# Kernel optimization log

Hardware: AMD Instinct MI355X
Metric: run time of the kernel (lower is better)

The kernel has to match this reference:

```python
import jax, jax.numpy as jnp
import numpy as np

N = 50000
E = 800000
H = 128

def setup_inputs() -> dict:
    key = jax.random.key(0)
    ks = jax.random.split(key, 12)
    s = 1.0 / np.sqrt(H)
    inp = {
        "x": jax.random.normal(ks[0], (N, H), dtype=jnp.float32),
        "edge_index": jax.random.randint(ks[1], (2, E), 0, N, dtype=jnp.int64),
        "edge_attr": jax.random.normal(ks[2], (E, H), dtype=jnp.float32),
        # linear_edge: Linear(3H, H)
        "We": jax.random.uniform(ks[3], (3 * H, H), jnp.float32, -s, s),
        "be": jnp.zeros((H,), jnp.float32),
        # attention_layer.W: Linear(H, H)
        "Wg": jax.random.uniform(ks[4], (H, H), jnp.float32, -s, s),
        "bg": jnp.zeros((H,), jnp.float32),
        # attention_layer.a: Linear(2H, 1)
        "Wa": jax.random.uniform(ks[5], (2 * H, 1), jnp.float32, -s, s),
        "ba": jnp.zeros((1,), jnp.float32),
        # linear_out: Linear(H, H)
        "Wo": jax.random.uniform(ks[6], (H, H), jnp.float32, -s, s),
        "bo": jnp.zeros((H,), jnp.float32),
    }
    return inp


def reference(x, edge_index, edge_attr, We, be, Wg, bg, Wa, ba, Wo, bo):
    # PyG MessagePassing (flow=source_to_target): j = edge_index[0] (source),
    # i = edge_index[1] (target); aggregation scatters to edge_index[1].
    src = edge_index[0]
    dst = edge_index[1]

    # message: SiLU(Linear(cat[x_i, x_j, edge_attr]))  -- split We to avoid a [E,3H] concat
    m = jax.nn.silu(x[dst] @ We[:H] + x[src] @ We[H:2 * H] + edge_attr @ We[2 * H:] + be)  # [E,H]
    agg = jax.ops.segment_sum(m, dst, num_segments=N)  # [N,H] scatter-add aggregate

    # GraphAttentionLayer: row, col = edge_index -> row=edge_index[0], col=edge_index[1]
    h = agg @ Wg + bg  # [N,H]
    score = jax.nn.leaky_relu(h[src] @ Wa[:H] + h[dst] @ Wa[H:] + ba, negative_slope=0.2)  # [E,1]
    # softmax over the last dim of size 1 -> all ones (faithful to original); dropout off (eval)
    alpha = jax.nn.softmax(score, axis=-1)  # [E,1]
    attn_out = jax.ops.segment_sum(alpha * h[dst], src, num_segments=N)  # [N,H]

    return attn_out @ Wo + bo  # linear_out
```

## Files before the change

### kernel.cpp

```cpp
#include <hip/hip_runtime.h>

#define N_NODES 50000
#define N_EDGES 800000
#define N_TILES 50000

typedef unsigned short u16;
typedef unsigned int u32;
typedef __attribute__((ext_vector_type(8))) short short8;
typedef __attribute__((ext_vector_type(4))) float f32x4;
typedef __attribute__((ext_vector_type(2))) float f32x2;

__device__ __forceinline__ u16 f2bf(float f) {
    union { float f; u32 u; } v; v.f = f;
    u32 r = v.u + 0x7FFFu + ((v.u >> 16) & 1u);
    return (u16)(r >> 16);
}

__device__ __forceinline__ float bf2f(u16 h) {
    union { u32 u; float f; } v; v.u = ((u32)h) << 16;
    return v.f;
}

__global__ __launch_bounds__(256) void prep_kernel(const float* __restrict__ x,
                                                   const float* __restrict__ We,
                                                   const float* __restrict__ Wg,
                                                   const float* __restrict__ bg,
                                                   const float* __restrict__ Wo,
                                                   u16* __restrict__ Xbf,
                                                   u16* __restrict__ PBe,
                                                   u16* __restrict__ PBc,
                                                   float* __restrict__ bc,
                                                   float* __restrict__ aggF,
                                                   int* __restrict__ degZ) {
    int b = blockIdx.x, tid = threadIdx.x;
    if (b < 3125) {
        size_t i = ((size_t)b * 256 + tid) * 8;
        f32x4 v0 = *(const f32x4*)(x + i);
        f32x4 v1 = *(const f32x4*)(x + i + 4);
        short8 o;
#pragma unroll
        for (int j = 0; j < 4; ++j) { o[j] = (short)f2bf(v0[j]); o[4 + j] = (short)f2bf(v1[j]); }
        *(short8*)(Xbf + i) = o;
    } else if (b < 4725) {
        int bb = b - 3125;
#pragma unroll
        for (int k = 0; k < 4; ++k) {
            int idx4 = bb * 1024 + k * 256 + tid;
            if (idx4 < 1600000) ((f32x4*)aggF)[idx4] = (f32x4){0.f, 0.f, 0.f, 0.f};
        }
    } else if (b < 4823) {
        int idx4 = (b - 4725) * 256 + tid;
        if (idx4 < 25000) ((int4*)degZ)[idx4] = make_int4(0, 0, 0, 0);
    } else if (b < 4847) {
        int bb = b - 4823;
        int jb = bb >> 3, t = bb & 7;
        const float* src = (jb == 0) ? We + 32768 : (jb == 1) ? We + 16384 : We;
        int c = tid >> 6, lane = tid & 63, q = lane >> 4, n = lane & 15;
        int slot = jb * 4 + c;
        const float* s = src + (size_t)(c * 32 + q * 8) * 128 + t * 16 + n;
        u16* dp = PBe + (((size_t)(t * 12 + slot) * 64 + lane) * 8);
#pragma unroll
        for (int j = 0; j < 8; ++j) dp[j] = f2bf(s[(size_t)j * 128]);
    } else if (b < 4855) {
        int w = b - 4847;
        for (int i = 0; i < 8; ++i) {
            int o = w * 2048 + i * 256 + tid;
            int k = o >> 7, n = o & 127;
            float s = 0.f;
            for (int j = 0; j < 128; ++j) s += Wg[k * 128 + j] * Wo[j * 128 + n];
            int t = n >> 4, c = k >> 5, q = (k >> 3) & 3, j8 = k & 7;
            int ln = (q << 4) | (n & 15);
            PBc[(((size_t)(t * 4 + c) * 64 + ln) * 8) + j8] = f2bf(s);
        }
    } else {
        if (tid < 128) {
            float s = 0.f;
            for (int j = 0; j < 128; ++j) s += bg[j] * Wo[j * 128 + tid];
            bc[tid] = s;
        }
    }
}

__global__ __launch_bounds__(256) void hist_kernel(const int* __restrict__ srcIdx,
                                                   const int* __restrict__ dstIdx,
                                                   int* __restrict__ degD,
                                                   int* __restrict__ degS) {
    int e = blockIdx.x * 256 + threadIdx.x;
    if (e >= N_EDGES) return;
    atomicAdd(&degD[dstIdx[e]], 1);
    atomicAdd(&degS[srcIdx[e]], 1);
}

__global__ __launch_bounds__(256) void scan_kernel(const int* __restrict__ degD,
                                                   const int* __restrict__ degS,
                                                   int* __restrict__ offD, int* __restrict__ curD,
                                                   int* __restrict__ offS, int* __restrict__ curS) {
    const int* deg = blockIdx.x ? degS : degD;
    int* off = blockIdx.x ? offS : offD;
    int* cur = blockIdx.x ? curS : curD;
    __shared__ int buf[256];
    const int CHUNK = 196;
    int tid = threadIdx.x;
    int s0 = tid * CHUNK, s1 = s0 + CHUNK;
    if (s1 > N_NODES) s1 = N_NODES;
    int s = 0;
    for (int i = s0; i < s1; ++i) s += deg[i];
    buf[tid] = s;
    __syncthreads();
    for (int o = 1; o < 256; o <<= 1) {
        int v = (tid >= o) ? buf[tid - o] : 0;
        __syncthreads();
        buf[tid] += v;
        __syncthreads();
    }
    int run = (tid > 0) ? buf[tid - 1] : 0;
    for (int i = s0; i < s1; ++i) {
        off[i] = run;
        cur[i] = run;
        run += deg[i];
    }
    if (tid == 255) off[N_NODES] = buf[255];
}

__global__ __launch_bounds__(256) void scatter_kernel(const int* __restrict__ srcIdx,
                                                      const int* __restrict__ dstIdx,
                                                      int* __restrict__ curD,
                                                      int* __restrict__ curS,
                                                      int4* __restrict__ sdP,
                                                      int* __restrict__ ss_dst) {
    int e = blockIdx.x * 256 + threadIdx.x;
    if (e >= N_EDGES) return;
    int s = srcIdx[e], d = dstIdx[e];
    int p = atomicAdd(&curD[d], 1);
    sdP[p] = make_int4(e, s, d, 0);
    int p2 = atomicAdd(&curS[s], 1);
    ss_dst[p2] = d;
}

__global__ __launch_bounds__(256) void gemm_mfma(const float* __restrict__ Ap,
                                                 const u16* __restrict__ PB,
                                                 const float* __restrict__ bias,
                                                 const float* __restrict__ bias2,
                                                 const int* __restrict__ rowdeg,
                                                 float* __restrict__ outp,
                                                 int M, int Ctiles) {
    int tid = threadIdx.x;
    int wave = tid >> 6;
    int lane = tid & 63;
    int strip = blockIdx.x * 4 + wave;
    int row0 = strip * 16;
    if (row0 >= M) return;
    int q = lane >> 4, n = lane & 15;
    int C = Ctiles * 16;

    short8 a[4];
    const float* ap = Ap + (size_t)(row0 + n) * 128 + q * 8;
#pragma unroll
    for (int c = 0; c < 4; ++c) {
        f32x4 f0 = *(const f32x4*)(ap + c * 32);
        f32x4 f1 = *(const f32x4*)(ap + c * 32 + 4);
        short8 t;
#pragma unroll
        for (int j = 0; j < 4; ++j) {
            t[j] = (short)f2bf(f0[j]);
            t[4 + j] = (short)f2bf(f1[j]);
        }
        a[c] = t;
    }

    float rb[4];
#pragma unroll
    for (int r = 0; r < 4; ++r) rb[r] = (float)rowdeg[row0 + q * 4 + r];

    for (int t = 0; t < Ctiles; ++t) {
        f32x4 acc = {0.f, 0.f, 0.f, 0.f};
#pragma unroll
        for (int c = 0; c < 4; ++c) {
            short8 b = *(const short8*)(PB + (((size_t)t * 4 + c) * 64 + lane) * 8);
            acc = __builtin_amdgcn_mfma_f32_16x16x32_bf16(a[c], b, acc, 0, 0, 0);
        }
        int col = t * 16 + n;
        float bv = bias[col];
        float b2 = bias2[col];
#pragma unroll
        for (int r = 0; r < 4; ++r) {
            int row = row0 + q * 4 + r;
            outp[(size_t)row * C + col] = acc[r] + bv + rb[r] * b2;
        }
    }
}

__global__ __launch_bounds__(256) void agg_fused(const float* __restrict__ EA,
                                                 const u16* __restrict__ Xbf,
                                                 const u16* __restrict__ PBe,
                                                 const float* __restrict__ be,
                                                 const int4* __restrict__ sdP,
                                                 float* __restrict__ aggF) {
    int tid = threadIdx.x;
    int wave = tid >> 6;
    int lane = tid & 63;
    int tile = blockIdx.x * 4 + wave;
    int q = lane >> 4, n = lane & 15;

    int4 es = sdP[tile * 16 + n];
    const float* ap = EA + (size_t)es.x * 128 + q * 8;
    const u16* xs = Xbf + (size_t)es.y * 128 + q * 8;
    const u16* xd = Xbf + (size_t)es.z * 128 + q * 8;

    short8 a[12];
#pragma unroll
    for (int c = 0; c < 4; ++c) {
        f32x4 f0 = *(const f32x4*)(ap + c * 32);
        f32x4 f1 = *(const f32x4*)(ap + c * 32 + 4);
        short8 t;
#pragma unroll
        for (int j = 0; j < 4; ++j) {
            t[j] = (short)f2bf(f0[j]);
            t[4 + j] = (short)f2bf(f1[j]);
        }
        a[c] = t;
        a[4 + c] = *(const short8*)(xs + c * 32);
        a[8 + c] = *(const short8*)(xd + c * 32);
    }

    int d0 = __shfl(es.z, q * 4 + 0, 64);
    int d1 = __shfl(es.z, q * 4 + 1, 64);
    int d2 = __shfl(es.z, q * 4 + 2, 64);
    int d3 = __shfl(es.z, q * 4 + 3, 64);
    bool c1 = (d1 == d0), c2 = (d2 == d1), c3 = (d3 == d2);

    float bb[8];
#pragma unroll
    for (int t = 0; t < 8; ++t) bb[t] = be[t * 16 + n];

#pragma unroll
    for (int t = 0; t < 8; ++t) {
        f32x4 acc = {0.f, 0.f, 0.f, 0.f};
#pragma unroll
        for (int c = 0; c < 12; ++c) {
            short8 b = *(const short8*)(PBe + (((size_t)t * 12 + c) * 64 + lane) * 8);
            acc = __builtin_amdgcn_mfma_f32_16x16x32_bf16(a[c], b, acc, 0, 0, 0);
        }
        float v0 = acc[0] + bb[t], v1 = acc[1] + bb[t], v2 = acc[2] + bb[t], v3 = acc[3] + bb[t];
        v0 *= __builtin_amdgcn_rcpf(1.f + __expf(-v0));
        v1 *= __builtin_amdgcn_rcpf(1.f + __expf(-v1));
        v2 *= __builtin_amdgcn_rcpf(1.f + __expf(-v2));
        v3 *= __builtin_amdgcn_rcpf(1.f + __expf(-v3));
        float s0 = v0;
        float s1 = v1 + (c1 ? s0 : 0.f);
        float s2 = v2 + (c2 ? s1 : 0.f);
        float s3 = v3 + (c3 ? s2 : 0.f);
        float* basep = aggF + t * 16 + n;
        if (!c1) atomicAdd(basep + (size_t)d0 * 128, s0);
        if (!c2) atomicAdd(basep + (size_t)d1 * 128, s1);
        if (!c3) atomicAdd(basep + (size_t)d2 * 128, s2);
        atomicAdd(basep + (size_t)d3 * 128, s3);
    }
}

__global__ __launch_bounds__(256) void attn_gather(const int* __restrict__ offS,
                                                   const int* __restrict__ ss_dst,
                                                   const float* __restrict__ aggF,
                                                   float* __restrict__ attnB) {
    int tid = threadIdx.x;
    int wave = tid >> 6;
    int lane = tid & 63;
    int node = blockIdx.x * 4 + wave;
    if (node >= N_NODES) return;
    int e0 = offS[node], e1 = offS[node + 1];
    float a0 = 0.f, a1 = 0.f;
    for (int base = e0; base < e1; base += 16) {
        int m = e1 - base;
        if (m > 16) m = 16;
        int ii = base + (lane & 15);
        if (ii > e1 - 1) ii = e1 - 1;
        int idxv = ss_dst[ii];
#pragma unroll
        for (int i = 0; i < 16; ++i) {
            bool val = i < m;
            int d = __shfl(idxv, val ? i : 0, 64);
            f32x2 h = *(const f32x2*)(aggF + (size_t)d * 128 + lane * 2);
            a0 += val ? h[0] : 0.f;
            a1 += val ? h[1] : 0.f;
        }
    }
    f32x2 o;
    o[0] = a0;
    o[1] = a1;
    *(f32x2*)(attnB + (size_t)node * 128 + lane * 2) = o;
}

extern "C" void kernel_launch(void* const* d_in, const int* in_sizes, int n_in,
                              void* d_out, int out_size, void* d_ws, size_t ws_size,
                              hipStream_t stream) {
    const float* x  = (const float*)d_in[0];
    const int* ei   = (const int*)d_in[1];
    const float* ea = (const float*)d_in[2];
    const float* We = (const float*)d_in[3];
    const float* be = (const float*)d_in[4];
    const float* Wg = (const float*)d_in[5];
    const float* bg = (const float*)d_in[6];
    const float* Wo = (const float*)d_in[9];
    const float* bo = (const float*)d_in[10];
    float* out = (float*)d_out;

    const int* srcIdx = ei;
    const int* dstIdx = ei + N_EDGES;

    char* ws = (char*)d_ws;
    u16*   PBe    = (u16*)(ws + 0);
    u16*   PBc    = (u16*)(ws + 98304);
    float* bc     = (float*)(ws + 131072);
    u16*   Xbf    = (u16*)(ws + 262144);
    int4*  sdP    = (int4*)(ws + 13062144);
    float* attnB  = (float*)(ws + 262144);
    int*   ss_dst = (int*)(ws + 25862144);
    float* aggF   = (float*)(ws + 29062144);
    int*   degD   = (int*)(ws + 54662144);
    int*   degS   = (int*)(ws + 54862144);
    int*   offD   = (int*)(ws + 55062144);
    int*   offS   = (int*)(ws + 55262160);
    int*   curD   = (int*)(ws + 55462176);
    int*   curS   = (int*)(ws + 55662176);

    prep_kernel<<<4856, 256, 0, stream>>>(x, We, Wg, bg, Wo, Xbf, PBe, PBc, bc, aggF, degD);

    hist_kernel<<<3125, 256, 0, stream>>>(srcIdx, dstIdx, degD, degS);
    scan_kernel<<<2, 256, 0, stream>>>(degD, degS, offD, curD, offS, curS);
    scatter_kernel<<<3125, 256, 0, stream>>>(srcIdx, dstIdx, curD, curS, sdP, ss_dst);

    agg_fused<<<12500, 256, 0, stream>>>(ea, Xbf, PBe, be, sdP, aggF);

    attn_gather<<<12500, 256, 0, stream>>>(offS, ss_dst, aggF, attnB);

    gemm_mfma<<<782, 256, 0, stream>>>(attnB, PBc, bo, bc, degS, out, N_NODES, 8);

    (void)in_sizes; (void)n_in; (void)out_size; (void)ws_size;
}
```

Before: 1.230 ms.

## Reorder output GEMM before gather, restructure edge aggregation with register-resident weights

Moves the combined node GEMM ahead of the source-side gather so it runs on aggregated features, and applies biases (scaled by degree) inside the gather kernel. The edge aggregation kernel now has each wave keep two output column tiles of weights in registers and loop over 8 edge tiles, with XCD-aware block remapping and cross-quad segment merging to reduce atomics. The scan kernel is vectorized with int4 loads and stores. Trade-offs: higher register pressure from 24 resident B fragments, and four waves per block now recompute the same A fragments for different column tiles.

Result: faster. 1.165 ms (-5.3%).

```diff
diff --git a/kernel.cpp b/kernel.cpp
--- a/kernel.cpp
+++ b/kernel.cpp
@@ -103,8 +103,13 @@
     int tid = threadIdx.x;
     int s0 = tid * CHUNK, s1 = s0 + CHUNK;
     if (s1 > N_NODES) s1 = N_NODES;
+    int i40 = s0 >> 2, i41 = s1 >> 2;
+    const int4* deg4 = (const int4*)deg;
     int s = 0;
-    for (int i = s0; i < s1; ++i) s += deg[i];
+    for (int i = i40; i < i41; ++i) {
+        int4 v = deg4[i];
+        s += v.x + v.y + v.z + v.w;
+    }
     buf[tid] = s;
     __syncthreads();
     for (int o = 1; o < 256; o <<= 1) {
@@ -114,10 +119,16 @@
         __syncthreads();
     }
     int run = (tid > 0) ? buf[tid - 1] : 0;
-    for (int i = s0; i < s1; ++i) {
-        off[i] = run;
-        cur[i] = run;
-        run += deg[i];
+    for (int i = i40; i < i41; ++i) {
+        int4 v = deg4[i];
+        int4 o;
+        o.x = run;
+        o.y = o.x + v.x;
+        o.z = o.y + v.y;
+        o.w = o.z + v.z;
+        ((int4*)off)[i] = o;
+        ((int4*)cur)[i] = o;
+        run = o.w + v.w;
     }
     if (tid == 255) off[N_NODES] = buf[255];
 }
@@ -139,11 +150,8 @@
 
 __global__ __launch_bounds__(256) void gemm_mfma(const float* __restrict__ Ap,
                                                  const u16* __restrict__ PB,
-                                                 const float* __restrict__ bias,
-                                                 const float* __restrict__ bias2,
-                                                 const int* __restrict__ rowdeg,
                                                  float* __restrict__ outp,
-                                                 int M, int Ctiles) {
+                                                 int M) {
     int tid = threadIdx.x;
     int wave = tid >> 6;
     int lane = tid & 63;
@@ -151,7 +159,6 @@
     int row0 = strip * 16;
     if (row0 >= M) return;
     int q = lane >> 4, n = lane & 15;
-    int C = Ctiles * 16;
 
     short8 a[4];
     const float* ap = Ap + (size_t)(row0 + n) * 128 + q * 8;
@@ -168,11 +175,7 @@
         a[c] = t;
     }
 
-    float rb[4];
-#pragma unroll
-    for (int r = 0; r < 4; ++r) rb[r] = (float)rowdeg[row0 + q * 4 + r];
-
-    for (int t = 0; t < Ctiles; ++t) {
+    for (int t = 0; t < 8; ++t) {
         f32x4 acc = {0.f, 0.f, 0.f, 0.f};
 #pragma unroll
         for (int c = 0; c < 4; ++c) {
@@ -180,12 +183,10 @@
             acc = __builtin_amdgcn_mfma_f32_16x16x32_bf16(a[c], b, acc, 0, 0, 0);
         }
         int col = t * 16 + n;
-        float bv = bias[col];
-        float b2 = bias2[col];
 #pragma unroll
         for (int r = 0; r < 4; ++r) {
             int row = row0 + q * 4 + r;
-            outp[(size_t)row * C + col] = acc[r] + bv + rb[r] * b2;
+            outp[(size_t)row * 128 + col] = acc[r];
         }
     }
 }
@@ -199,69 +200,97 @@
     int tid = threadIdx.x;
     int wave = tid >> 6;
     int lane = tid & 63;
-    int tile = blockIdx.x * 4 + wave;
     int q = lane >> 4, n = lane & 15;
 
-    int4 es = sdP[tile * 16 + n];
-    const float* ap = EA + (size_t)es.x * 128 + q * 8;
-    const u16* xs = Xbf + (size_t)es.y * 128 + q * 8;
-    const u16* xd = Xbf + (size_t)es.z * 128 + q * 8;
-
-    short8 a[12];
-#pragma unroll
-    for (int c = 0; c < 4; ++c) {
-        f32x4 f0 = *(const f32x4*)(ap + c * 32);
-        f32x4 f1 = *(const f32x4*)(ap + c * 32 + 4);
-        short8 t;
-#pragma unroll
-        for (int j = 0; j < 4; ++j) {
-            t[j] = (short)f2bf(f0[j]);
-            t[4 + j] = (short)f2bf(f1[j]);
-        }
-        a[c] = t;
-        a[4 + c] = *(const short8*)(xs + c * 32);
-        a[8 + c] = *(const short8*)(xd + c * 32);
-    }
-
-    int d0 = __shfl(es.z, q * 4 + 0, 64);
-    int d1 = __shfl(es.z, q * 4 + 1, 64);
-    int d2 = __shfl(es.z, q * 4 + 2, 64);
-    int d3 = __shfl(es.z, q * 4 + 3, 64);
-    bool c1 = (d1 == d0), c2 = (d2 == d1), c3 = (d3 == d2);
-
-    float bb[8];
-#pragma unroll
-    for (int t = 0; t < 8; ++t) bb[t] = be[t * 16 + n];
-
-#pragma unroll
-    for (int t = 0; t < 8; ++t) {
-        f32x4 acc = {0.f, 0.f, 0.f, 0.f};
-#pragma unroll
-        for (int c = 0; c < 12; ++c) {
-            short8 b = *(const short8*)(PBe + (((size_t)t * 12 + c) * 64 + lane) * 8);
-            acc = __builtin_amdgcn_mfma_f32_16x16x32_bf16(a[c], b, acc, 0, 0, 0);
-        }
-        float v0 = acc[0] + bb[t], v1 = acc[1] + bb[t], v2 = acc[2] + bb[t], v3 = acc[3] + bb[t];
-        v0 *= __builtin_amdgcn_rcpf(1.f + __expf(-v0));
-        v1 *= __builtin_amdgcn_rcpf(1.f + __expf(-v1));
-        v2 *= __builtin_amdgcn_rcpf(1.f + __expf(-v2));
-        v3 *= __builtin_amdgcn_rcpf(1.f + __expf(-v3));
-        float s0 = v0;
-        float s1 = v1 + (c1 ? s0 : 0.f);
-        float s2 = v2 + (c2 ? s1 : 0.f);
-        float s3 = v3 + (c3 ? s2 : 0.f);
-        float* basep = aggF + t * 16 + n;
-        if (!c1) atomicAdd(basep + (size_t)d0 * 128, s0);
-        if (!c2) atomicAdd(basep + (size_t)d1 * 128, s1);
-        if (!c3) atomicAdd(basep + (size_t)d2 * 128, s2);
-        atomicAdd(basep + (size_t)d3 * 128, s3);
-    }
-}
-
-__global__ __launch_bounds__(256) void attn_gather(const int* __restrict__ offS,
-                                                   const int* __restrict__ ss_dst,
-                                                   const float* __restrict__ aggF,
-                                                   float* __restrict__ attnB) {
+    int bid = blockIdx.x;
+    int xcd = bid & 7, pos = bid >> 3;
+    int blk = (xcd < 2 ? xcd * 782 : 1564 + (xcd - 2) * 781) + pos;
+    int tileBase = blk * 8;
+
+    int t0 = wave * 2;
+    short8 B[24];
+#pragma unroll
+    for (int tt = 0; tt < 2; ++tt)
+#pragma unroll
+        for (int c = 0; c < 12; ++c)
+            B[tt * 12 + c] = *(const short8*)(PBe + (((size_t)(t0 + tt) * 12 + c) * 64 + lane) * 8);
+    float bb[2] = {be[t0 * 16 + n], be[t0 * 16 + 16 + n]};
+
+    for (int s = 0; s < 8; ++s) {
+        int tile = tileBase + s;
+        int4 es = sdP[tile * 16 + n];
+        const float* ap = EA + (size_t)es.x * 128 + q * 8;
+        const u16* xs = Xbf + (size_t)es.y * 128 + q * 8;
+        const u16* xd = Xbf + (size_t)es.z * 128 + q * 8;
+
+        short8 a[12];
+#pragma unroll
+        for (int c = 0; c < 4; ++c) {
+            f32x4 f0 = *(const f32x4*)(ap + c * 32);
+            f32x4 f1 = *(const f32x4*)(ap + c * 32 + 4);
+            short8 t;
+#pragma unroll
+            for (int j = 0; j < 4; ++j) {
+                t[j] = (short)f2bf(f0[j]);
+                t[4 + j] = (short)f2bf(f1[j]);
+            }
+            a[c] = t;
+            a[4 + c] = *(const short8*)(xs + c * 32);
+            a[8 + c] = *(const short8*)(xd + c * 32);
+        }
+
+        int d0 = __shfl(es.z, q * 4 + 0, 64);
+        int d1 = __shfl(es.z, q * 4 + 1, 64);
+        int d2 = __shfl(es.z, q * 4 + 2, 64);
+        int d3 = __shfl(es.z, q * 4 + 3, 64);
+        bool c1 = (d1 == d0), c2 = (d2 == d1), c3 = (d3 == d2);
+        bool m1 = c1, m2 = c1 && c2, m3 = m2 && c3;
+        int dp = __shfl(d3, lane - 16, 64);
+        int dn = __shfl(d0, lane + 16, 64);
+        bool contPrev = (q > 0) && (d0 == dp);
+        bool flush3 = (q == 3) || (d3 != dn);
+
+#pragma unroll
+        for (int tt = 0; tt < 2; ++tt) {
+            f32x4 acc = {0.f, 0.f, 0.f, 0.f};
+#pragma unroll
+            for (int c = 0; c < 12; ++c)
+                acc = __builtin_amdgcn_mfma_f32_16x16x32_bf16(a[c], B[tt * 12 + c], acc, 0, 0, 0);
+            float v0 = acc[0] + bb[tt], v1 = acc[1] + bb[tt];
+            float v2 = acc[2] + bb[tt], v3 = acc[3] + bb[tt];
+            v0 *= __builtin_amdgcn_rcpf(1.f + __expf(-v0));
+            v1 *= __builtin_amdgcn_rcpf(1.f + __expf(-v1));
+            v2 *= __builtin_amdgcn_rcpf(1.f + __expf(-v2));
+            v3 *= __builtin_amdgcn_rcpf(1.f + __expf(-v3));
+            float s0 = v0;
+            float s1 = v1 + (c1 ? s0 : 0.f);
+            float s2 = v2 + (c2 ? s1 : 0.f);
+            float s3 = v3 + (c3 ? s2 : 0.f);
+            float carry = 0.f;
+#pragma unroll
+            for (int it = 0; it < 3; ++it) {
+                float ps = __shfl(s3 + (m3 ? carry : 0.f), lane - 16, 64);
+                carry = contPrev ? ps : 0.f;
+            }
+            s0 += carry;
+            s1 += m1 ? carry : 0.f;
+            s2 += m2 ? carry : 0.f;
+            s3 += m3 ? carry : 0.f;
+            float* basep = aggF + (t0 + tt) * 16 + n;
+            if (!c1) atomicAdd(basep + (size_t)d0 * 128, s0);
+            if (!c2) atomicAdd(basep + (size_t)d1 * 128, s1);
+            if (!c3) atomicAdd(basep + (size_t)d2 * 128, s2);
+            if (flush3) atomicAdd(basep + (size_t)d3 * 128, s3);
+        }
+    }
+}
+
+__global__ __launch_bounds__(256) void out_gather(const int* __restrict__ offS,
+                                                  const int* __restrict__ ss_dst,
+                                                  const float* __restrict__ aggW,
+                                                  const float* __restrict__ bc,
+                                                  const float* __restrict__ bo,
+                                                  float* __restrict__ out) {
     int tid = threadIdx.x;
     int wave = tid >> 6;
     int lane = tid & 63;
@@ -279,15 +308,16 @@
         for (int i = 0; i < 16; ++i) {
             bool val = i < m;
             int d = __shfl(idxv, val ? i : 0, 64);
-            f32x2 h = *(const f32x2*)(aggF + (size_t)d * 128 + lane * 2);
+            f32x2 h = *(const f32x2*)(aggW + (size_t)d * 128 + lane * 2);
             a0 += val ? h[0] : 0.f;
             a1 += val ? h[1] : 0.f;
         }
     }
+    float deg = (float)(e1 - e0);
     f32x2 o;
-    o[0] = a0;
-    o[1] = a1;
-    *(f32x2*)(attnB + (size_t)node * 128 + lane * 2) = o;
+    o[0] = a0 + deg * bc[lane * 2] + bo[lane * 2];
+    o[1] = a1 + deg * bc[lane * 2 + 1] + bo[lane * 2 + 1];
+    *(f32x2*)(out + (size_t)node * 128 + lane * 2) = o;
 }
 
 extern "C" void kernel_launch(void* const* d_in, const int* in_sizes, int n_in,
@@ -313,7 +343,7 @@
     float* bc     = (float*)(ws + 131072);
     u16*   Xbf    = (u16*)(ws + 262144);
     int4*  sdP    = (int4*)(ws + 13062144);
-    float* attnB  = (float*)(ws + 262144);
+    float* aggW   = (float*)(ws + 262144);
     int*   ss_dst = (int*)(ws + 25862144);
     float* aggF   = (float*)(ws + 29062144);
     int*   degD   = (int*)(ws + 54662144);
@@ -329,11 +359,11 @@
     scan_kernel<<<2, 256, 0, stream>>>(degD, degS, offD, curD, offS, curS);
     scatter_kernel<<<3125, 256, 0, stream>>>(srcIdx, dstIdx, curD, curS, sdP, ss_dst);
 
-    agg_fused<<<12500, 256, 0, stream>>>(ea, Xbf, PBe, be, sdP, aggF);
-
-    attn_gather<<<12500, 256, 0, stream>>>(offS, ss_dst, aggF, attnB);
-
-    gemm_mfma<<<782, 256, 0, stream>>>(attnB, PBc, bo, bc, degS, out, N_NODES, 8);
+    agg_fused<<<6250, 256, 0, stream>>>(ea, Xbf, PBe, be, sdP, aggF);
+
+    gemm_mfma<<<782, 256, 0, stream>>>(aggF, PBc, aggW, N_NODES);
+
+    out_gather<<<12500, 256, 0, stream>>>(offS, ss_dst, aggW, bc, bo, out);
 
     (void)in_sizes; (void)n_in; (void)out_size; (void)ws_size;
 }
```
